# Optimization experiments

Measured on AMD Instinct MI355X. Metric: run time of the kernel, lower is better.

Reference implementation:

```python
import jax, jax.numpy as jnp
import numpy as np

V = 100000   # vocab (emb_size == stoich_size so all 8 branches index safely)
D = 256      # emb_dimension
S = 128      # stoich_dimension
H = 512      # hidden_size
B = 8192     # batch of skip-gram pairs
K = 32       # negative samples per pair
NUM_REGULAR = 60000  # num_regular_words


def _mlp(x, w1, b1, w2, b2):
    # Sequential(Linear(S,H), ReLU, Linear(H,D))
    return jax.nn.relu(x @ w1 + b1) @ w2 + b2


def setup_inputs() -> dict:
    key = jax.random.key(0)
    k = jax.random.split(key, 14)
    initrange = 1.0 / D
    return {
        "pos_u": jax.random.randint(k[0], (B,), 0, V),
        "pos_v": jax.random.randint(k[1], (B,), 0, V),
        "neg_v": jax.random.randint(k[2], (B, K), 0, V),
        "u_emb": jax.random.uniform(k[3], (V, D), jnp.float32, -initrange, initrange),
        "v_emb": jax.random.normal(k[4], (V, D), jnp.float32) * 0.01,
        "stoich": jax.random.uniform(k[5], (V, S), jnp.float32),
        "tw1": jax.random.normal(k[6], (S, H), jnp.float32) * 0.05,
        "tb1": jnp.zeros((H,), jnp.float32),
        "tw2": jax.random.normal(k[7], (H, D), jnp.float32) * 0.05,
        "tb2": jnp.zeros((D,), jnp.float32),
        "cw1": jax.random.normal(k[8], (S, H), jnp.float32) * 0.05,
        "cb1": jnp.zeros((H,), jnp.float32),
        "cw2": jax.random.normal(k[9], (H, D), jnp.float32) * 0.05,
        "cb2": jnp.zeros((D,), jnp.float32),
    }


def _masked_score(emb_u, emb_v, emb_neg_v, u_mask, v_mask, neg_v_mask):
    # pos: [B]
    pos = jnp.clip(jnp.sum(emb_u * emb_v, axis=1), -10.0, 10.0)
    pos = jnp.where(v_mask, 0.0, -jax.nn.log_sigmoid(pos))
    # neg: [B,K] = bmm(emb_neg_v [B,K,D], emb_u [B,D,1])
    neg = jnp.clip(jnp.einsum("bkd,bd->bk", emb_neg_v, emb_u), -10.0, 10.0)
    ls = jnp.where(neg_v_mask, 0.0, jax.nn.log_sigmoid(-neg))
    neg_score = -jnp.sum(ls, axis=1)
    return jnp.where(u_mask, 0.0, pos + neg_score)


def reference(pos_u, pos_v, neg_v, u_emb, v_emb, stoich,
              tw1, tb1, tw2, tb2, cw1, cb1, cw2, cb2):
    emb_u_w = u_emb[pos_u]                 # [B,D]
    emb_v_w = v_emb[pos_v]                 # [B,D]
    emb_neg_v_w = v_emb[neg_v]             # [B,K,D]
    emb_u_m = _mlp(stoich[pos_u], tw1, tb1, tw2, tb2)       # [B,D]
    emb_v_m = _mlp(stoich[pos_v], cw1, cb1, cw2, cb2)       # [B,D]
    emb_neg_v_m = _mlp(stoich[neg_v], cw1, cb1, cw2, cb2)   # [B,K,D]

    u_pairs = [(emb_u_w, pos_u >= NUM_REGULAR), (emb_u_m, pos_u < NUM_REGULAR)]
    v_pairs = [(emb_v_w, pos_v >= NUM_REGULAR), (emb_v_m, pos_v < NUM_REGULAR)]
    n_pairs = [(emb_neg_v_w, neg_v >= NUM_REGULAR), (emb_neg_v_m, neg_v < NUM_REGULAR)]

    total = jnp.zeros((B,), emb_u_w.dtype)
    for eu, um in u_pairs:
        for ev, vm in v_pairs:
            for env, nm in n_pairs:
                total = total + _masked_score(eu, ev, env, um, vm, nm)
    return jnp.mean(total)
```

## Files before the change

kernel.cpp:

```cpp
#include <hip/hip_runtime.h>
#include <hip/hip_bf16.h>
#include <math.h>

#define V_SIZE 100000
#define D_DIM  256
#define S_DIM  128
#define H_DIM  512
#define B_SIZE 8192
#define K_NEG  32
#define NR     60000
#define NMOD   (V_SIZE - NR)

typedef __attribute__((ext_vector_type(8))) short bf16x8;
typedef __attribute__((ext_vector_type(4))) float f32x4;

static __device__ __forceinline__ short f2bf(float f) {
    unsigned u = __builtin_bit_cast(unsigned, f);
    unsigned r = (u + 0x7fffu + ((u >> 16) & 1u)) >> 16;
    return (short)r;
}

__global__ __launch_bounds__(256) void convert_x_kernel(
    const float* __restrict__ stoich, short* __restrict__ xbf)
{
    int t4 = blockIdx.x * 256 + threadIdx.x;
    const float4 v = ((const float4*)(stoich + (size_t)NR * S_DIM))[t4];
    short4 o;
    o.x = f2bf(v.x); o.y = f2bf(v.y); o.z = f2bf(v.z); o.w = f2bf(v.w);
    ((short4*)xbf)[t4] = o;
}

__global__ __launch_bounds__(256) void gather_xu_kernel(
    const float* __restrict__ stoich, const int* __restrict__ pos_u,
    short* __restrict__ xu)
{
    int t = blockIdx.x * 256 + threadIdx.x;
    int b = t >> 5, j = t & 31;
    int pu = pos_u[b];
    const float4 v = *(const float4*)(stoich + (size_t)pu * S_DIM + j * 4);
    short4 o;
    o.x = f2bf(v.x); o.y = f2bf(v.y); o.z = f2bf(v.z); o.w = f2bf(v.w);
    ((short4*)xu)[t] = o;
}

__global__ __launch_bounds__(256) void transpose_w_kernel(
    const float* __restrict__ in, short* __restrict__ out, int K, int N)
{
    int t = blockIdx.x * 256 + threadIdx.x;
    if (t >= K * N) return;
    int n = t / K, k = t - n * K;
    out[t] = f2bf(in[(size_t)k * N + n]);
}

#define TM 32
#define HPAD 528

__global__ __launch_bounds__(256, 2) void fused_mlp_kernel(
    const short* __restrict__ A,
    const short* __restrict__ W1T,
    const float* __restrict__ b1,
    const short* __restrict__ W2T,
    const float* __restrict__ b2,
    float* __restrict__ out)
{
    __shared__ short sH[TM * HPAD];

    const int lane = threadIdx.x & 63;
    const int wv   = threadIdx.x >> 6;
    const int m0   = blockIdx.x * TM;
    const int fr   = lane & 15;
    const int q    = lane >> 4;

    const short* Ap = A + (size_t)(m0 + fr) * S_DIM + q * 8;
    bf16x8 a[4][2];
    #pragma unroll
    for (int ks = 0; ks < 4; ++ks)
        #pragma unroll
        for (int mi = 0; mi < 2; ++mi)
            a[ks][mi] = *(const bf16x8*)(Ap + (size_t)mi * 16 * S_DIM + ks * 32);

    #pragma unroll
    for (int half = 0; half < 2; ++half) {
        const int n0h = wv * 128 + half * 64;
        const short* Bp = W1T + (size_t)(n0h + fr) * S_DIM + q * 8;
        f32x4 acc[2][4] = {};
        #pragma unroll
        for (int ks = 0; ks < 4; ++ks) {
            bf16x8 bfr[4];
            #pragma unroll
            for (int ni = 0; ni < 4; ++ni)
                bfr[ni] = *(const bf16x8*)(Bp + (size_t)ni * 16 * S_DIM + ks * 32);
            #pragma unroll
            for (int mi = 0; mi < 2; ++mi)
                #pragma unroll
                for (int ni = 0; ni < 4; ++ni)
                    acc[mi][ni] = __builtin_amdgcn_mfma_f32_16x16x32_bf16(
                        a[ks][mi], bfr[ni], acc[mi][ni], 0, 0, 0);
        }
        #pragma unroll
        for (int ni = 0; ni < 4; ++ni) {
            int c = n0h + ni * 16 + fr;
            float bv = b1[c];
            #pragma unroll
            for (int mi = 0; mi < 2; ++mi)
                #pragma unroll
                for (int r = 0; r < 4; ++r) {
                    int row = mi * 16 + q * 4 + r;
                    sH[row * HPAD + c] = f2bf(fmaxf(acc[mi][ni][r] + bv, 0.f));
                }
        }
    }
    __syncthreads();

    f32x4 acc2[2][4] = {};
    const short* B2p = W2T + (size_t)(wv * 64 + fr) * H_DIM + q * 8;
    #pragma unroll 4
    for (int ks = 0; ks < 16; ++ks) {
        bf16x8 a2[2], b2f[4];
        #pragma unroll
        for (int mi = 0; mi < 2; ++mi)
            a2[mi] = *(const bf16x8*)(&sH[(mi * 16 + fr) * HPAD + q * 8 + ks * 32]);
        #pragma unroll
        for (int ni = 0; ni < 4; ++ni)
            b2f[ni] = *(const bf16x8*)(B2p + (size_t)ni * 16 * H_DIM + ks * 32);
        #pragma unroll
        for (int mi = 0; mi < 2; ++mi)
            #pragma unroll
            for (int ni = 0; ni < 4; ++ni)
                acc2[mi][ni] = __builtin_amdgcn_mfma_f32_16x16x32_bf16(
                    a2[mi], b2f[ni], acc2[mi][ni], 0, 0, 0);
    }
    #pragma unroll
    for (int ni = 0; ni < 4; ++ni) {
        int c = wv * 64 + ni * 16 + fr;
        float bv = b2[c];
        #pragma unroll
        for (int mi = 0; mi < 2; ++mi)
            #pragma unroll
            for (int r = 0; r < 4; ++r) {
                int row = m0 + mi * 16 + q * 4 + r;
                out[(size_t)row * D_DIM + c] = acc2[mi][ni][r] + bv;
            }
    }
}

__device__ __forceinline__ float logsig_fast(float x) {
    float t = __expf(-fabsf(x));
    return fminf(x, 0.f) - __logf(1.f + t);
}
__device__ __forceinline__ float clip10(float x) {
    return fminf(fmaxf(x, -10.f), 10.f);
}
__device__ __forceinline__ float dot4(float4 a, float4 b) {
    return a.x * b.x + a.y * b.y + a.z * b.z + a.w * b.w;
}

__global__ __launch_bounds__(256) void score_kernel(
    const int*   __restrict__ pos_u,
    const int*   __restrict__ pos_v,
    const int*   __restrict__ neg_v,
    const float* __restrict__ u_emb,
    const float* __restrict__ v_emb,
    const float* __restrict__ tab_c,
    const float* __restrict__ Ubuf,
    float* __restrict__ partials)
{
    const int b    = blockIdx.x;
    const int lane = threadIdx.x & 63;
    const int wv   = threadIdx.x >> 6;
    const int g    = lane >> 4;
    const int l    = lane & 15;

    int pu = pos_u[b];
    const float* eup = (pu < NR) ? u_emb + (size_t)pu * D_DIM
                                 : Ubuf  + (size_t)b  * D_DIM;
    float4 eu[4];
    #pragma unroll
    for (int j = 0; j < 4; ++j)
        eu[j] = *(const float4*)(eup + l * 16 + j * 4);

    float part = 0.f;
    const int* nv = neg_v + (size_t)b * K_NEG + wv * 8;

    #pragma unroll
    for (int it = 0; it < 2; ++it) {
        int ix = nv[it * 4 + g];
        const float* rp = (ix < NR) ? v_emb + (size_t)ix * D_DIM
                                    : tab_c + (size_t)(ix - NR) * D_DIM;
        float d = 0.f;
        #pragma unroll
        for (int j = 0; j < 4; ++j)
            d += dot4(eu[j], *(const float4*)(rp + l * 16 + j * 4));
        #pragma unroll
        for (int o = 1; o < 16; o <<= 1) d += __shfl_xor(d, o, 64);
        part -= logsig_fast(-clip10(d));
    }

    if (wv == 0) {
        int pv = pos_v[b];
        const float* rp = (pv < NR) ? v_emb + (size_t)pv * D_DIM
                                    : tab_c + (size_t)(pv - NR) * D_DIM;
        float d = 0.f;
        #pragma unroll
        for (int j = 0; j < 4; ++j)
            d += dot4(eu[j], *(const float4*)(rp + l * 16 + j * 4));
        #pragma unroll
        for (int o = 1; o < 16; o <<= 1) d += __shfl_xor(d, o, 64);
        float term = -logsig_fast(clip10(d));
        if (g == 0) part += term;
    }

    float ws = part;
    #pragma unroll
    for (int o = 32; o; o >>= 1) ws += __shfl_xor(ws, o, 64);
    __shared__ float sp[4];
    if (lane == 0) sp[wv] = ws * 0.0625f;
    __syncthreads();
    if (threadIdx.x == 0)
        partials[b] = sp[0] + sp[1] + sp[2] + sp[3];
}

__global__ __launch_bounds__(256) void reduce_kernel(
    const float* __restrict__ partials, float* __restrict__ out)
{
    float s = 0.f;
    for (int i = threadIdx.x; i < B_SIZE; i += 256) s += partials[i];
    #pragma unroll
    for (int o = 32; o; o >>= 1) s += __shfl_xor(s, o, 64);
    __shared__ float sp[4];
    if ((threadIdx.x & 63) == 0) sp[threadIdx.x >> 6] = s;
    __syncthreads();
    if (threadIdx.x == 0)
        out[0] = (sp[0] + sp[1] + sp[2] + sp[3]) * (2.0f / (float)B_SIZE);
}

extern "C" void kernel_launch(void* const* d_in, const int* in_sizes, int n_in,
                              void* d_out, int out_size, void* d_ws, size_t ws_size,
                              hipStream_t stream) {
    const int*   pos_u  = (const int*)  d_in[0];
    const int*   pos_v  = (const int*)  d_in[1];
    const int*   neg_v  = (const int*)  d_in[2];
    const float* u_emb  = (const float*)d_in[3];
    const float* v_emb  = (const float*)d_in[4];
    const float* stoich = (const float*)d_in[5];
    const float* tw1    = (const float*)d_in[6];
    const float* tb1    = (const float*)d_in[7];
    const float* tw2    = (const float*)d_in[8];
    const float* tb2    = (const float*)d_in[9];
    const float* cw1    = (const float*)d_in[10];
    const float* cb1    = (const float*)d_in[11];
    const float* cw2    = (const float*)d_in[12];
    const float* cb2    = (const float*)d_in[13];
    float* out = (float*)d_out;

    char* ws = (char*)d_ws;
    short* Xbf   = (short*)(ws);
    short* Xu    = (short*)(ws + 10240000);
    short* W1T_t = (short*)(ws + 12337152);
    short* W1T_c = (short*)(ws + 12468224);
    short* W2T_t = (short*)(ws + 12599296);
    short* W2T_c = (short*)(ws + 12861440);
    float* tab_c = (float*)(ws + 13123584);
    float* Ubuf  = (float*)(ws + 54083584);
    float* parts = (float*)(ws + 62472192);

    dim3 blk(256);

    convert_x_kernel<<<dim3(NMOD * S_DIM / 4 / 256), blk, 0, stream>>>(stoich, Xbf);
    gather_xu_kernel<<<dim3(B_SIZE * S_DIM / 4 / 256), blk, 0, stream>>>(stoich, pos_u, Xu);
    transpose_w_kernel<<<dim3((S_DIM * H_DIM + 255) / 256), blk, 0, stream>>>(tw1, W1T_t, S_DIM, H_DIM);
    transpose_w_kernel<<<dim3((S_DIM * H_DIM + 255) / 256), blk, 0, stream>>>(cw1, W1T_c, S_DIM, H_DIM);
    transpose_w_kernel<<<dim3((H_DIM * D_DIM + 255) / 256), blk, 0, stream>>>(tw2, W2T_t, H_DIM, D_DIM);
    transpose_w_kernel<<<dim3((H_DIM * D_DIM + 255) / 256), blk, 0, stream>>>(cw2, W2T_c, H_DIM, D_DIM);

    fused_mlp_kernel<<<dim3(B_SIZE / TM), blk, 0, stream>>>(Xu,  W1T_t, tb1, W2T_t, tb2, Ubuf);
    fused_mlp_kernel<<<dim3(NMOD  / TM), blk, 0, stream>>>(Xbf, W1T_c, cb1, W2T_c, cb2, tab_c);

    score_kernel<<<dim3(B_SIZE), blk, 0, stream>>>(pos_u, pos_v, neg_v,
                                                   u_emb, v_emb, tab_c, Ubuf, parts);
    reduce_kernel<<<dim3(1), blk, 0, stream>>>(parts, out);
}
```

Baseline: 359.8 us.

## Merge MLP launches into one grid, enlarge row tile, prefetch second GEMM

Merges the two MLP launches (context table and target batch) into a single grid that picks its operands by block index. It also merges the four weight transposes into one launch. The row tile grows from 32 to 48, with inputs padded and zero-filled to tile multiples and workspace offsets moved to match. The second GEMM now double-buffers its LDS and weight fragment loads, and the shared-memory padding changes. The aim is less launch overhead, better tail balance and more reuse of weight fragments, at the cost of higher register pressure (launch bounds now ask for 3 blocks per SM) and possible LDS bank conflicts from the new padding.

```diff
diff --git a/kernel.cpp b/kernel.cpp
--- a/kernel.cpp
+++ b/kernel.cpp
@@ -11,6 +11,13 @@
 #define NR     60000
 #define NMOD   (V_SIZE - NR)
 
+#define TM     48
+#define CBLK   834
+#define UBLK   171
+#define MC_PAD (CBLK * TM)
+#define MU_PAD (UBLK * TM)
+#define HPAD   516
+
 typedef __attribute__((ext_vector_type(8))) short bf16x8;
 typedef __attribute__((ext_vector_type(4))) float f32x4;
 
@@ -24,9 +31,11 @@
     const float* __restrict__ stoich, short* __restrict__ xbf)
 {
     int t4 = blockIdx.x * 256 + threadIdx.x;
-    const float4 v = ((const float4*)(stoich + (size_t)NR * S_DIM))[t4];
-    short4 o;
-    o.x = f2bf(v.x); o.y = f2bf(v.y); o.z = f2bf(v.z); o.w = f2bf(v.w);
+    short4 o = {0, 0, 0, 0};
+    if (t4 < NMOD * S_DIM / 4) {
+        const float4 v = ((const float4*)(stoich + (size_t)NR * S_DIM))[t4];
+        o.x = f2bf(v.x); o.y = f2bf(v.y); o.z = f2bf(v.z); o.w = f2bf(v.w);
+    }
     ((short4*)xbf)[t4] = o;
 }
 
@@ -36,106 +45,146 @@
 {
     int t = blockIdx.x * 256 + threadIdx.x;
     int b = t >> 5, j = t & 31;
-    int pu = pos_u[b];
-    const float4 v = *(const float4*)(stoich + (size_t)pu * S_DIM + j * 4);
-    short4 o;
-    o.x = f2bf(v.x); o.y = f2bf(v.y); o.z = f2bf(v.z); o.w = f2bf(v.w);
+    short4 o = {0, 0, 0, 0};
+    if (b < B_SIZE) {
+        int pu = pos_u[b];
+        const float4 v = *(const float4*)(stoich + (size_t)pu * S_DIM + j * 4);
+        o.x = f2bf(v.x); o.y = f2bf(v.y); o.z = f2bf(v.z); o.w = f2bf(v.w);
+    }
     ((short4*)xu)[t] = o;
 }
 
-__global__ __launch_bounds__(256) void transpose_w_kernel(
-    const float* __restrict__ in, short* __restrict__ out, int K, int N)
+__global__ __launch_bounds__(256) void transpose_all_kernel(
+    const float* __restrict__ tw1, const float* __restrict__ cw1,
+    const float* __restrict__ tw2, const float* __restrict__ cw2,
+    short* __restrict__ W1T_t, short* __restrict__ W1T_c,
+    short* __restrict__ W2T_t, short* __restrict__ W2T_c)
 {
     int t = blockIdx.x * 256 + threadIdx.x;
-    if (t >= K * N) return;
-    int n = t / K, k = t - n * K;
-    out[t] = f2bf(in[(size_t)k * N + n]);
-}
-
-#define TM 32
-#define HPAD 528
-
-__global__ __launch_bounds__(256, 2) void fused_mlp_kernel(
-    const short* __restrict__ A,
-    const short* __restrict__ W1T,
-    const float* __restrict__ b1,
-    const short* __restrict__ W2T,
-    const float* __restrict__ b2,
-    float* __restrict__ out)
+    if (t < 65536) {
+        int n = t >> 7, k = t & 127;
+        W1T_t[t] = f2bf(tw1[(size_t)k * H_DIM + n]);
+    } else if (t < 131072) {
+        int t2 = t - 65536; int n = t2 >> 7, k = t2 & 127;
+        W1T_c[t2] = f2bf(cw1[(size_t)k * H_DIM + n]);
+    } else if (t < 262144) {
+        int t2 = t - 131072; int n = t2 >> 9, k = t2 & 511;
+        W2T_t[t2] = f2bf(tw2[(size_t)k * D_DIM + n]);
+    } else {
+        int t2 = t - 262144; int n = t2 >> 9, k = t2 & 511;
+        W2T_c[t2] = f2bf(cw2[(size_t)k * D_DIM + n]);
+    }
+}
+
+__global__ __launch_bounds__(256, 3) void fused_mlp_kernel(
+    const short* __restrict__ Xc,  const short* __restrict__ W1c,
+    const float* __restrict__ b1c, const short* __restrict__ W2c,
+    const float* __restrict__ b2c, float* __restrict__ outc,
+    const short* __restrict__ Xu,  const short* __restrict__ W1u,
+    const float* __restrict__ b1u, const short* __restrict__ W2u,
+    const float* __restrict__ b2u, float* __restrict__ outu)
 {
     __shared__ short sH[TM * HPAD];
+
+    const int blk = blockIdx.x;
+    const short *A, *W1T, *W2T; const float *b1, *b2; float* out; int m0;
+    if (blk < CBLK) { A = Xc; W1T = W1c; b1 = b1c; W2T = W2c; b2 = b2c;
+                      out = outc; m0 = blk * TM; }
+    else            { A = Xu; W1T = W1u; b1 = b1u; W2T = W2u; b2 = b2u;
+                      out = outu; m0 = (blk - CBLK) * TM; }
 
     const int lane = threadIdx.x & 63;
     const int wv   = threadIdx.x >> 6;
-    const int m0   = blockIdx.x * TM;
     const int fr   = lane & 15;
     const int q    = lane >> 4;
 
     const short* Ap = A + (size_t)(m0 + fr) * S_DIM + q * 8;
-    bf16x8 a[4][2];
+    bf16x8 af[4][3];
     #pragma unroll
     for (int ks = 0; ks < 4; ++ks)
         #pragma unroll
-        for (int mi = 0; mi < 2; ++mi)
-            a[ks][mi] = *(const bf16x8*)(Ap + (size_t)mi * 16 * S_DIM + ks * 32);
+        for (int mi = 0; mi < 3; ++mi)
+            af[ks][mi] = *(const bf16x8*)(Ap + mi * 16 * S_DIM + ks * 32);
 
     #pragma unroll
     for (int half = 0; half < 2; ++half) {
         const int n0h = wv * 128 + half * 64;
         const short* Bp = W1T + (size_t)(n0h + fr) * S_DIM + q * 8;
-        f32x4 acc[2][4] = {};
+        f32x4 acc[3][4] = {};
         #pragma unroll
         for (int ks = 0; ks < 4; ++ks) {
             bf16x8 bfr[4];
             #pragma unroll
             for (int ni = 0; ni < 4; ++ni)
-                bfr[ni] = *(const bf16x8*)(Bp + (size_t)ni * 16 * S_DIM + ks * 32);
-            #pragma unroll
-            for (int mi = 0; mi < 2; ++mi)
+                bfr[ni] = *(const bf16x8*)(Bp + ni * 16 * S_DIM + ks * 32);
+            #pragma unroll
+            for (int mi = 0; mi < 3; ++mi)
                 #pragma unroll
                 for (int ni = 0; ni < 4; ++ni)
                     acc[mi][ni] = __builtin_amdgcn_mfma_f32_16x16x32_bf16(
-                        a[ks][mi], bfr[ni], acc[mi][ni], 0, 0, 0);
+                        af[ks][mi], bfr[ni], acc[mi][ni], 0, 0, 0);
         }
         #pragma unroll
         for (int ni = 0; ni < 4; ++ni) {
             int c = n0h + ni * 16 + fr;
             float bv = b1[c];
             #pragma unroll
-            for (int mi = 0; mi < 2; ++mi)
+            for (int mi = 0; mi < 3; ++mi)
                 #pragma unroll
-                for (int r = 0; r < 4; ++r) {
-                    int row = mi * 16 + q * 4 + r;
-                    sH[row * HPAD + c] = f2bf(fmaxf(acc[mi][ni][r] + bv, 0.f));
-                }
+                for (int r = 0; r < 4; ++r)
+                    sH[(mi * 16 + q * 4 + r) * HPAD + c] =
+                        f2bf(fmaxf(acc[mi][ni][r] + bv, 0.f));
         }
     }
     __syncthreads();
 
-    f32x4 acc2[2][4] = {};
-    const short* B2p = W2T + (size_t)(wv * 64 + fr) * H_DIM + q * 8;
-    #pragma unroll 4
+    const short* Bp2 = W2T + (size_t)(wv * 64 + fr) * H_DIM + q * 8;
+    f32x4 acc2[3][4] = {};
+    bf16x8 bcur[4], bnxt[4], acur[3], anxt[3];
+
+    #define LOAD_B(ks, dst)                                                   \
+        _Pragma("unroll")                                                     \
+        for (int ni = 0; ni < 4; ++ni)                                        \
+            dst[ni] = *(const bf16x8*)(Bp2 + ni * 16 * H_DIM + (ks) * 32);
+    #define LOAD_A(ks, dst)                                                   \
+        _Pragma("unroll")                                                     \
+        for (int mi = 0; mi < 3; ++mi) {                                      \
+            const short* hp = &sH[(mi * 16 + fr) * HPAD + (ks) * 32 + q * 8]; \
+            short4 lo = *(const short4*)hp;                                   \
+            short4 hi = *(const short4*)(hp + 4);                             \
+            bf16x8 v;                                                         \
+            v[0] = lo.x; v[1] = lo.y; v[2] = lo.z; v[3] = lo.w;               \
+            v[4] = hi.x; v[5] = hi.y; v[6] = hi.z; v[7] = hi.w;               \
+            dst[mi] = v;                                                      \
+        }
+
+    LOAD_B(0, bcur);
+    LOAD_A(0, acur);
+    #pragma unroll
     for (int ks = 0; ks < 16; ++ks) {
-        bf16x8 a2[2], b2f[4];
-        #pragma unroll
-        for (int mi = 0; mi < 2; ++mi)
-            a2[mi] = *(const bf16x8*)(&sH[(mi * 16 + fr) * HPAD + q * 8 + ks * 32]);
-        #pragma unroll
-        for (int ni = 0; ni < 4; ++ni)
-            b2f[ni] = *(const bf16x8*)(B2p + (size_t)ni * 16 * H_DIM + ks * 32);
-        #pragma unroll
-        for (int mi = 0; mi < 2; ++mi)
+        if (ks < 15) { LOAD_B(ks + 1, bnxt); LOAD_A(ks + 1, anxt); }
+        #pragma unroll
+        for (int mi = 0; mi < 3; ++mi)
             #pragma unroll
             for (int ni = 0; ni < 4; ++ni)
                 acc2[mi][ni] = __builtin_amdgcn_mfma_f32_16x16x32_bf16(
-                    a2[mi], b2f[ni], acc2[mi][ni], 0, 0, 0);
-    }
+                    acur[mi], bcur[ni], acc2[mi][ni], 0, 0, 0);
+        if (ks < 15) {
+            #pragma unroll
+            for (int i = 0; i < 4; ++i) bcur[i] = bnxt[i];
+            #pragma unroll
+            for (int i = 0; i < 3; ++i) acur[i] = anxt[i];
+        }
+    }
+    #undef LOAD_A
+    #undef LOAD_B
+
     #pragma unroll
     for (int ni = 0; ni < 4; ++ni) {
         int c = wv * 64 + ni * 16 + fr;
         float bv = b2[c];
         #pragma unroll
-        for (int mi = 0; mi < 2; ++mi)
+        for (int mi = 0; mi < 3; ++mi)
             #pragma unroll
             for (int r = 0; r < 4; ++r) {
                 int row = m0 + mi * 16 + q * 4 + r;
@@ -255,26 +304,25 @@
 
     char* ws = (char*)d_ws;
     short* Xbf   = (short*)(ws);
-    short* Xu    = (short*)(ws + 10240000);
-    short* W1T_t = (short*)(ws + 12337152);
-    short* W1T_c = (short*)(ws + 12468224);
-    short* W2T_t = (short*)(ws + 12599296);
-    short* W2T_c = (short*)(ws + 12861440);
-    float* tab_c = (float*)(ws + 13123584);
-    float* Ubuf  = (float*)(ws + 54083584);
-    float* parts = (float*)(ws + 62472192);
+    short* Xu    = (short*)(ws + 10248192);
+    short* W1T_t = (short*)(ws + 12349440);
+    short* W1T_c = (short*)(ws + 12480512);
+    short* W2T_t = (short*)(ws + 12611584);
+    short* W2T_c = (short*)(ws + 12873728);
+    float* tab_c = (float*)(ws + 13135872);
+    float* Ubuf  = (float*)(ws + 54128640);
+    float* parts = (float*)(ws + 62533632);
 
     dim3 blk(256);
 
-    convert_x_kernel<<<dim3(NMOD * S_DIM / 4 / 256), blk, 0, stream>>>(stoich, Xbf);
-    gather_xu_kernel<<<dim3(B_SIZE * S_DIM / 4 / 256), blk, 0, stream>>>(stoich, pos_u, Xu);
-    transpose_w_kernel<<<dim3((S_DIM * H_DIM + 255) / 256), blk, 0, stream>>>(tw1, W1T_t, S_DIM, H_DIM);
-    transpose_w_kernel<<<dim3((S_DIM * H_DIM + 255) / 256), blk, 0, stream>>>(cw1, W1T_c, S_DIM, H_DIM);
-    transpose_w_kernel<<<dim3((H_DIM * D_DIM + 255) / 256), blk, 0, stream>>>(tw2, W2T_t, H_DIM, D_DIM);
-    transpose_w_kernel<<<dim3((H_DIM * D_DIM + 255) / 256), blk, 0, stream>>>(cw2, W2T_c, H_DIM, D_DIM);
-
-    fused_mlp_kernel<<<dim3(B_SIZE / TM), blk, 0, stream>>>(Xu,  W1T_t, tb1, W2T_t, tb2, Ubuf);
-    fused_mlp_kernel<<<dim3(NMOD  / TM), blk, 0, stream>>>(Xbf, W1T_c, cb1, W2T_c, cb2, tab_c);
+    convert_x_kernel<<<dim3(MC_PAD * S_DIM / 4 / 256), blk, 0, stream>>>(stoich, Xbf);
+    gather_xu_kernel<<<dim3(MU_PAD * S_DIM / 4 / 256), blk, 0, stream>>>(stoich, pos_u, Xu);
+    transpose_all_kernel<<<dim3(393216 / 256), blk, 0, stream>>>(
+        tw1, cw1, tw2, cw2, W1T_t, W1T_c, W2T_t, W2T_c);
+
+    fused_mlp_kernel<<<dim3(CBLK + UBLK), blk, 0, stream>>>(
+        Xbf, W1T_c, cb1, W2T_c, cb2, tab_c,
+        Xu,  W1T_t, tb1, W2T_t, tb2, Ubuf);
 
     score_kernel<<<dim3(B_SIZE), blk, 0, stream>>>(pos_u, pos_v, neg_v,
                                                    u_emb, v_emb, tab_c, Ubuf, parts);
```

Result: faster. 324.1 us (-9.9%).
